# Kernel optimization log

Hardware: AMD Instinct MI355X
Metric: run time of the kernel (lower is better)

## Reference

```python
import jax, jax.numpy as jnp
import numpy as np

# RRFU config (matches init_kwargs)
S = 2          # scale_factor
G = 4          # groups
K = 3          # sample_k
C = 64         # in_channels
B, H, W_IN = 4, 128, 128
SC = S * S     # s_c
KC = K * K     # sample_c (3x3 = 9)


def setup_inputs() -> dict:
    key = jax.random.key(0)
    ks = jax.random.split(key, 9)
    x = jax.random.normal(ks[0], (B, C, H, W_IN), jnp.float32)
    # 1x1 conv weights stored as (out_ch, in_ch); std chosen per module's init
    # (mask convs are zero-init in the original; use small random so math is nontrivial)
    w_off = jax.random.normal(ks[1], (G * SC * 2, C), jnp.float32) * 0.001
    b_off = jnp.zeros((G * SC * 2,), jnp.float32)
    w_offm = jax.random.normal(ks[2], (G * SC * 2, C), jnp.float32) * 0.01
    b_offm = jnp.zeros((G * SC * 2,), jnp.float32)
    w_sk = jax.random.normal(ks[3], (KC, C), jnp.float32) * 0.005
    b_sk = jnp.zeros((KC,), jnp.float32)
    w_km = jax.random.normal(ks[4], (KC, C), jnp.float32) * 0.01
    b_km = jnp.zeros((KC,), jnp.float32)
    return {"x": x, "w_off": w_off, "b_off": b_off, "w_offm": w_offm,
            "b_offm": b_offm, "w_sk": w_sk, "b_sk": b_sk, "w_km": w_km, "b_km": b_km}


def _conv1x1(x, w, b):
    return jnp.einsum('oc,bchw->bohw', w, x) + b[None, :, None, None]


def _bilinear_border(img, iy, ix):
    """img: (Cg,H,W); iy,ix: (Ho,Wo) pixel coords. grid_sample bilinear, padding_mode='border'."""
    Hh, Ww = img.shape[1], img.shape[2]
    ix = jnp.clip(ix, 0.0, Ww - 1.0)
    iy = jnp.clip(iy, 0.0, Hh - 1.0)
    x0 = jnp.floor(ix)
    y0 = jnp.floor(iy)
    wx = ix - x0
    wy = iy - y0
    x0i = x0.astype(jnp.int32)
    y0i = y0.astype(jnp.int32)
    x1i = jnp.minimum(x0i + 1, Ww - 1)
    y1i = jnp.minimum(y0i + 1, Hh - 1)
    v00 = img[:, y0i, x0i]
    v01 = img[:, y0i, x1i]
    v10 = img[:, y1i, x0i]
    v11 = img[:, y1i, x1i]
    return (v00 * (1 - wx) * (1 - wy) + v01 * wx * (1 - wy)
            + v10 * (1 - wx) * wy + v11 * wx * wy)


def reference(x, w_off, b_off, w_offm, b_offm, w_sk, b_sk, w_km, b_km):
    b0, c0, h0, w0 = x.shape
    # learned offsets, gated by sigmoid mask
    off = _conv1x1(x, w_off, b_off) * jax.nn.sigmoid(_conv1x1(x, w_offm, b_offm))
    bg = b0 * G
    # (b, g*S*S*2, h, w) -> (bg, S, S, 2, h, w) -> (bg, h, S, w, S, 2) -> (bg, S*h, S*w, 2)
    off = off.reshape(bg, S, S, 2, h0, w0).transpose(0, 4, 1, 5, 2, 3).reshape(bg, S * h0, S * w0, 2)
    Ho, Wo = S * h0, S * w0
    # coord_base + offset, normalized then un-normalized for align_corners=False grid_sample
    cx = jnp.arange(Wo, dtype=x.dtype) + 0.5
    cy = jnp.arange(Ho, dtype=x.dtype) + 0.5
    ix = (cx[None, None, :] + off[..., 0]) * (w0 / Wo) - 0.5  # (bg, Ho, Wo)
    iy = (cy[None, :, None] + off[..., 1]) * (h0 / Ho) - 0.5
    x_r = x.reshape(bg, c0 // G, h0, w0)
    x_def = jax.vmap(_bilinear_border)(x_r, iy, ix).reshape(b0, c0, Ho, Wo)
    # CARAFE-style dynamic reassembly: softmax kernel over 3x3 neighborhood
    sk = _conv1x1(x_def, w_sk, b_sk) * jax.nn.sigmoid(_conv1x1(x_def, w_km, b_km))
    skn = jax.nn.softmax(sk, axis=1)  # (b, 9, Ho, Wo)
    pad = K // 2
    xp = jnp.pad(x_def, ((0, 0), (0, 0), (pad, pad), (pad, pad)))  # zero pad like F.unfold
    out = jnp.zeros_like(x_def)
    for ky in range(K):  # fixed 3x3 taps; avoids materializing (b,c,9,Ho,Wo)
        for kx in range(K):
            out = out + skn[:, ky * K + kx][:, None] * xp[:, :, ky:ky + Ho, kx:kx + Wo]
    return out
```

## Files before the change

kernel.cpp:

```cpp
#include <hip/hip_runtime.h>
#include <hip/hip_fp16.h>

typedef _Float16 h2 __attribute__((ext_vector_type(2)));

constexpr int Bc  = 4;
constexpr int Cc  = 64;
constexpr int H0  = 128;
constexpr int W0  = 128;
constexpr int HW  = H0 * W0;
constexpr int Gc  = 4;
constexpr int HOc = H0 * 2;
constexpr int WOc = W0 * 2;

constexpr int TW = 16;
constexpr int TH = 8;
constexpr int HX = TW + 2;
constexpr int HY = TH + 2;
constexpr int NHALO = HX * HY;
constexpr int NTASK = Gc * NHALO;

constexpr int SXC = 10;
constexpr int SYC = 6;
constexpr int SN  = SXC * SYC;
constexpr int NPAIR = Cc / 2;

union hu32 { unsigned u; h2 h; };

__device__ __forceinline__ float dot2(h2 a, unsigned bw, float c) {
    hu32 cv; cv.u = bw;
#if __has_builtin(__builtin_amdgcn_fdot2)
    return __builtin_amdgcn_fdot2(a, cv.h, c, false);
#else
    return fmaf((float)a[0], (float)cv.h[0],
                fmaf((float)a[1], (float)cv.h[1], c));
#endif
}

__global__ __launch_bounds__(256) void kT_prep(
    const float* __restrict__ w_off, const float* __restrict__ w_offm,
    const float* __restrict__ w_sk,  const float* __restrict__ w_km,
    __half2* __restrict__ wpk0, __half2* __restrict__ wpk)
{
    const int i = blockIdx.x * 256 + threadIdx.x;
    if (i < 2048) {
        const int c2  = i >> 6;
        const int rem = i & 63;
        const int mat = rem >> 5;
        const int r   = rem & 31;
        const float* src = mat ? w_offm : w_off;
        wpk0[i] = __floats2half2_rn(src[r * Cc + 2 * c2],
                                    src[r * Cc + 2 * c2 + 1]);
    } else if (i < 2048 + 576) {
        const int j   = i - 2048;
        const int mat = j >= 288;
        const int jj  = mat ? j - 288 : j;
        const int k   = jj >> 5;
        const int c2  = jj & 31;
        const float* src = mat ? w_km : w_sk;
        wpk[j] = __floats2half2_rn(src[k * Cc + 2 * c2],
                                   src[k * Cc + 2 * c2 + 1]);
    }
}

__global__ __launch_bounds__(256) void k0_offsets(
    const float* __restrict__ x, const unsigned* __restrict__ wpk0,
    const float* __restrict__ b_off, const float* __restrict__ b_offm,
    __half2* __restrict__ offbuf, unsigned* __restrict__ xt)
{
    const int b    = blockIdx.y;
    const int t    = threadIdx.x;
    const int wave = t >> 6, lane = t & 63;
    const int r0   = __builtin_amdgcn_readfirstlane(wave * 8);
    const int px   = blockIdx.x * 64 + lane;

    float a[8], m[8];
#pragma unroll
    for (int q = 0; q < 8; ++q) { a[q] = 0.f; m[q] = 0.f; }
    unsigned xtr[NPAIR];

    const float*    xp = x + (size_t)b * Cc * HW + px;
    const unsigned* wp = wpk0 + r0;

#pragma unroll 4
    for (int c2 = 0; c2 < NPAIR; ++c2) {
        const float x0 = xp[(2 * c2)     * HW];
        const float x1 = xp[(2 * c2 + 1) * HW];
        hu32 xh; xh.h = h2{(_Float16)x0, (_Float16)x1};
        xtr[c2] = xh.u;
#pragma unroll
        for (int q = 0; q < 8; ++q) {
            a[q] = dot2(xh.h, wp[c2 * 64 + q],      a[q]);
            m[q] = dot2(xh.h, wp[c2 * 64 + 32 + q], m[q]);
        }
    }

    __half2* ob = offbuf + ((size_t)b * HW + px) * 16 + (r0 >> 1);
#pragma unroll
    for (int j = 0; j < 4; ++j) {
        const int r = r0 + 2 * j;
        const float sx = 1.f / (1.f + __expf(-(m[2 * j]     + b_offm[r])));
        const float sy = 1.f / (1.f + __expf(-(m[2 * j + 1] + b_offm[r + 1])));
        const float vx = (a[2 * j]     + b_off[r])     * sx;
        const float vy = (a[2 * j + 1] + b_off[r + 1]) * sy;
        ob[j] = __floats2half2_rn(vx, vy);
    }

    if (wave == 0) {
        unsigned* xo = xt + ((size_t)b * HW + px) * NPAIR;
#pragma unroll
        for (int c2 = 0; c2 < NPAIR; ++c2) xo[c2] = xtr[c2];
    }
}

__global__ __launch_bounds__(256) void k1_fused(
    const unsigned* __restrict__ xt, const __half2* __restrict__ offbuf,
    const unsigned* __restrict__ wsku, const float* __restrict__ b_sk,
    const float* __restrict__ b_km,
    float* __restrict__ out)
{
    __shared__ h2    xd2[NPAIR][NHALO];
    __shared__ float ovl[2304];
    h2*       xstage2 = (h2*)ovl;
    float*    kmb     = ovl;
    unsigned* sknb    = (unsigned*)(ovl + 128 * 9);

    const unsigned* wkmu = wsku + 288;

    const int b    = blockIdx.y;
    const int tile = blockIdx.x;
    const int ox = (tile & 15) * TW;
    const int oy = (tile >> 4) * TH;
    const int t  = threadIdx.x;
    const int syr = (oy >> 1) - 1;
    const int sxr = (ox >> 1) - 1;

    const unsigned* xtb = xt + (size_t)b * HW * NPAIR;
    const __half2*  obb = offbuf + (size_t)b * HW * 16;

    unsigned* xs_u = (unsigned*)xstage2;
    for (int i = t; i < NPAIR * SN; i += 256) {
        const int c2  = i & 31;
        const int pos = i >> 5;
        const int r   = pos / SXC;
        const int j   = pos - r * SXC;
        const int yy  = min(max(syr + r, 0), H0 - 1);
        const int xx  = min(max(sxr + j, 0), W0 - 1);
        xs_u[c2 * SN + pos] = xtb[(yy * W0 + xx) * NPAIR + c2];
    }
    __syncthreads();

    for (int task = t; task < NTASK; task += 256) {
        const int g   = task / NHALO;
        const int pix = task - g * NHALO;
        const int hy  = pix / HX;
        const int hx  = pix - hy * HX;
        const int gy  = oy - 1 + hy;
        const int gx  = ox - 1 + hx;
        if (gy < 0 || gy >= HOc || gx < 0 || gx >= WOc) {
#pragma unroll
            for (int p = 0; p < 8; ++p) xd2[g * 8 + p][pix] = (h2)0;
            continue;
        }
        const int sy = gy & 1, sx = gx & 1;
        const int h  = gy >> 1, w  = gx >> 1;
        const __half2 o2 = obb[(size_t)(h * W0 + w) * 16 + g * 4 + sy * 2 + sx];
        const float offx = __low2float(o2);
        const float offy = __high2float(o2);

        float ix = ((float)gx + 0.5f + offx) * 0.5f - 0.5f;
        float iy = ((float)gy + 0.5f + offy) * 0.5f - 0.5f;
        ix = fminf(fmaxf(ix, 0.f), (float)(W0 - 1));
        iy = fminf(fmaxf(iy, 0.f), (float)(H0 - 1));
        const float x0f = floorf(ix), y0f = floorf(iy);
        const float wx = ix - x0f,   wy = iy - y0f;
        const int x0 = (int)x0f, y0 = (int)y0f;
        const int x1 = min(x0 + 1, W0 - 1), y1 = min(y0 + 1, H0 - 1);
        const float w00 = (1.f - wx) * (1.f - wy);
        const float w01 = wx * (1.f - wy);
        const float w10 = (1.f - wx) * wy;
        const float w11 = wx * wy;

        const int j0 = x0 - sxr, j1 = x1 - sxr;
        const int i0 = y0 - syr, i1 = y1 - syr;
        const bool inl = (j0 >= 0) & (j1 < SXC) & (i0 >= 0) & (i1 < SYC);

        const _Float16 W00 = (_Float16)w00, W01 = (_Float16)w01;
        const _Float16 W10 = (_Float16)w10, W11 = (_Float16)w11;

        if (inl) {
            const int o00 = i0 * SXC + j0, o01 = i0 * SXC + j1;
            const int o10 = i1 * SXC + j0, o11 = i1 * SXC + j1;
            const h2* s2 = xstage2 + (g * 8) * SN;
#pragma unroll
            for (int p = 0; p < 8; ++p) {
                const h2* pc = s2 + p * SN;
                xd2[g * 8 + p][pix] =
                    pc[o00] * W00 + pc[o01] * W01 + pc[o10] * W10 + pc[o11] * W11;
            }
        } else {
            const int o00 = (y0 * W0 + x0) * NPAIR, o01 = (y0 * W0 + x1) * NPAIR;
            const int o10 = (y1 * W0 + x0) * NPAIR, o11 = (y1 * W0 + x1) * NPAIR;
#pragma unroll
            for (int p = 0; p < 8; ++p) {
                const int c2 = g * 8 + p;
                hu32 v00, v01, v10, v11;
                v00.u = xtb[o00 + c2]; v01.u = xtb[o01 + c2];
                v10.u = xtb[o10 + c2]; v11.u = xtb[o11 + c2];
                xd2[c2][pix] =
                    v00.h * W00 + v01.h * W01 + v10.h * W10 + v11.h * W11;
            }
        }
    }
    __syncthreads();

    {
        const int p   = t & 127;
        const int ctr = ((p >> 4) + 1) * HX + (p & 15) + 1;
        h2 xv[NPAIR];
#pragma unroll
        for (int c2 = 0; c2 < NPAIR; ++c2) xv[c2] = xd2[c2][ctr];

        float acc[9];
        if (t < 128) {
#pragma unroll
            for (int k = 0; k < 9; ++k) {
                float a = 0.f;
#pragma unroll
                for (int c2 = 0; c2 < NPAIR; ++c2)
                    a = dot2(xv[c2], wsku[k * 32 + c2], a);
                acc[k] = a;
            }
        } else {
#pragma unroll
            for (int k = 0; k < 9; ++k) {
                float a = 0.f;
#pragma unroll
                for (int c2 = 0; c2 < NPAIR; ++c2)
                    a = dot2(xv[c2], wkmu[k * 32 + c2], a);
                kmb[p * 9 + k] = a;
            }
        }
        __syncthreads();

        if (t < 128) {
            float sv[9], mx = -1e30f;
#pragma unroll
            for (int k = 0; k < 9; ++k) {
                const float z = kmb[p * 9 + k] + b_km[k];
                sv[k] = (acc[k] + b_sk[k]) / (1.f + __expf(-z));
                mx = fmaxf(mx, sv[k]);
            }
            float sum = 0.f;
#pragma unroll
            for (int k = 0; k < 9; ++k) { sv[k] = __expf(sv[k] - mx); sum += sv[k]; }
            const float inv = 1.f / sum;
#pragma unroll
            for (int k = 0; k < 9; ++k) {
                const unsigned hu = __half_as_ushort(__float2half(sv[k] * inv));
                sknb[p * 9 + k] = hu | (hu << 16);
            }
        }
    }
    __syncthreads();

    {
        const int sq    = t & 31;
        const int chunk = t >> 5;
        const int sqx = sq & 7, sqy = sq >> 3;
        const int hx0 = 2 * sqx, hy0 = 2 * sqy;
        const int p00 = (2 * sqy) * TW + 2 * sqx;

        hu32 s00[9], s01[9], s10[9], s11[9];
#pragma unroll
        for (int k = 0; k < 9; ++k) {
            s00[k].u = sknb[p00 * 9 + k];        s01[k].u = sknb[(p00 + 1) * 9 + k];
            s10[k].u = sknb[(p00 + TW) * 9 + k]; s11[k].u = sknb[(p00 + TW + 1) * 9 + k];
        }
        const int orow0 = oy + 2 * sqy, ocol0 = ox + 2 * sqx;

#pragma unroll
        for (int i = 0; i < 4; ++i) {
            const int pr = chunk * 4 + i;
            h2 wd[4][4];
#pragma unroll
            for (int ry = 0; ry < 4; ++ry) {
                const int base = (hy0 + ry) * HX + hx0;
#pragma unroll
                for (int rx = 0; rx < 4; ++rx)
                    wd[ry][rx] = xd2[pr][base + rx];
            }
            h2 a00 = (h2)0, a01 = (h2)0, a10 = (h2)0, a11 = (h2)0;
#pragma unroll
            for (int ky = 0; ky < 3; ++ky)
#pragma unroll
                for (int kx = 0; kx < 3; ++kx) {
                    const int k = ky * 3 + kx;
                    a00 += s00[k].h * wd[ky    ][kx    ];
                    a01 += s01[k].h * wd[ky    ][kx + 1];
                    a10 += s10[k].h * wd[ky + 1][kx    ];
                    a11 += s11[k].h * wd[ky + 1][kx + 1];
                }
            float* ob0 = out + ((size_t)(b * Cc + 2 * pr)) * (HOc * WOc)
                             + (size_t)orow0 * WOc + ocol0;
            float* ob1 = ob0 + (size_t)(HOc * WOc);
            *reinterpret_cast<float2*>(ob0)       = make_float2((float)a00[0], (float)a01[0]);
            *reinterpret_cast<float2*>(ob0 + WOc) = make_float2((float)a10[0], (float)a11[0]);
            *reinterpret_cast<float2*>(ob1)       = make_float2((float)a00[1], (float)a01[1]);
            *reinterpret_cast<float2*>(ob1 + WOc) = make_float2((float)a10[1], (float)a11[1]);
        }
    }
}

extern "C" void kernel_launch(void* const* d_in, const int* in_sizes, int n_in,
                              void* d_out, int out_size, void* d_ws, size_t ws_size,
                              hipStream_t stream)
{
    const float* x      = (const float*)d_in[0];
    const float* w_off  = (const float*)d_in[1];
    const float* b_off  = (const float*)d_in[2];
    const float* w_offm = (const float*)d_in[3];
    const float* b_offm = (const float*)d_in[4];
    const float* w_sk   = (const float*)d_in[5];
    const float* b_sk   = (const float*)d_in[6];
    const float* w_km   = (const float*)d_in[7];
    const float* b_km   = (const float*)d_in[8];
    float* outp = (float*)d_out;

    const size_t off_bytes  = (size_t)Bc * HW * 16 * sizeof(__half2);
    const size_t xt_bytes   = (size_t)Bc * HW * NPAIR * sizeof(unsigned);
    const size_t wpk0_bytes = 2048 * sizeof(__half2);
    const size_t wpk_bytes  = 576 * sizeof(__half2);
    if (ws_size < off_bytes + xt_bytes + wpk0_bytes + wpk_bytes) return;
    __half2*  offbuf = (__half2*)d_ws;
    unsigned* xtbuf  = (unsigned*)((char*)d_ws + off_bytes);
    __half2*  wpk0   = (__half2*)((char*)d_ws + off_bytes + xt_bytes);
    __half2*  wpk    = (__half2*)((char*)d_ws + off_bytes + xt_bytes + wpk0_bytes);

    dim3 blk(256);
    hipLaunchKernelGGL(kT_prep, dim3(11), blk, 0, stream,
                       w_off, w_offm, w_sk, w_km, wpk0, wpk);

    dim3 g0(HW / 64, Bc);
    hipLaunchKernelGGL(k0_offsets, g0, blk, 0, stream,
                       x, (const unsigned*)wpk0, b_off, b_offm, offbuf, xtbuf);

    dim3 g1(512, Bc);
    hipLaunchKernelGGL(k1_fused, g1, blk, 0, stream,
                       xtbuf, offbuf, (const unsigned*)wpk, b_sk, b_km, outp);
}
```

Baseline: 60.71 us.

## Process two vertical tiles per block with register-prefetched staging of second tile

Each block of the fused kernel now handles two stacked 16x8 output tiles, halving the grid. The source staging data for both tiles is loaded into registers up front, and the second tile's copy is written to shared memory after the first tile's sampling phase, hiding global load latency. The staging buffer gets its own shared allocation instead of aliasing the softmax scratch, and the mask logits are kept in half precision. This adds register pressure (16 prefetch registers) and shared memory, which may reduce occupancy, and halves the number of blocks available for parallelism.

Result: faster. 55.43 us (-8.7%).

```diff
diff --git a/kernel.cpp b/kernel.cpp
--- a/kernel.cpp
+++ b/kernel.cpp
@@ -23,6 +23,7 @@
 constexpr int SYC = 6;
 constexpr int SN  = SXC * SYC;
 constexpr int NPAIR = Cc / 2;
+constexpr int NSTG  = NPAIR * SN;
 
 union hu32 { unsigned u; h2 h; };
 
@@ -118,196 +119,229 @@
     const float* __restrict__ b_km,
     float* __restrict__ out)
 {
-    __shared__ h2    xd2[NPAIR][NHALO];
-    __shared__ float ovl[2304];
-    h2*       xstage2 = (h2*)ovl;
-    float*    kmb     = ovl;
-    unsigned* sknb    = (unsigned*)(ovl + 128 * 9);
+    __shared__ h2       xd2[NPAIR][NHALO];
+    __shared__ unsigned xs_u[NSTG];
+    __shared__ unsigned short kmbh[128 * 9];
+    __shared__ unsigned sknb[128 * 9];
 
     const unsigned* wkmu = wsku + 288;
 
     const int b    = blockIdx.y;
-    const int tile = blockIdx.x;
-    const int ox = (tile & 15) * TW;
-    const int oy = (tile >> 4) * TH;
+    const int tp   = blockIdx.x;
+    const int ox = (tp & 15) * TW;
+    const int oyb = (tp >> 4) * (2 * TH);
     const int t  = threadIdx.x;
-    const int syr = (oy >> 1) - 1;
     const int sxr = (ox >> 1) - 1;
+    const int syr0 = (oyb >> 1) - 1;
+    const int syr1 = syr0 + (TH >> 1);
 
     const unsigned* xtb = xt + (size_t)b * HW * NPAIR;
     const __half2*  obb = offbuf + (size_t)b * HW * 16;
 
-    unsigned* xs_u = (unsigned*)xstage2;
-    for (int i = t; i < NPAIR * SN; i += 256) {
-        const int c2  = i & 31;
-        const int pos = i >> 5;
-        const int r   = pos / SXC;
-        const int j   = pos - r * SXC;
-        const int yy  = min(max(syr + r, 0), H0 - 1);
-        const int xx  = min(max(sxr + j, 0), W0 - 1);
-        xs_u[c2 * SN + pos] = xtb[(yy * W0 + xx) * NPAIR + c2];
+    unsigned pre0[8], pre1[8];
+#pragma unroll
+    for (int k = 0; k < 8; ++k) {
+        const int i = t + k * 256;
+        if (i < NSTG) {
+            const int c2  = i & 31;
+            const int pos = i >> 5;
+            const int r   = pos / SXC;
+            const int j   = pos - r * SXC;
+            const int xx  = min(max(sxr + j, 0), W0 - 1);
+            const int yy0 = min(max(syr0 + r, 0), H0 - 1);
+            const int yy1 = min(max(syr1 + r, 0), H0 - 1);
+            pre0[k] = xtb[(yy0 * W0 + xx) * NPAIR + c2];
+            pre1[k] = xtb[(yy1 * W0 + xx) * NPAIR + c2];
+        }
+    }
+#pragma unroll
+    for (int k = 0; k < 8; ++k) {
+        const int i = t + k * 256;
+        if (i < NSTG) {
+            const int c2 = i & 31, pos = i >> 5;
+            xs_u[c2 * SN + pos] = pre0[k];
+        }
     }
     __syncthreads();
 
-    for (int task = t; task < NTASK; task += 256) {
-        const int g   = task / NHALO;
-        const int pix = task - g * NHALO;
-        const int hy  = pix / HX;
-        const int hx  = pix - hy * HX;
-        const int gy  = oy - 1 + hy;
-        const int gx  = ox - 1 + hx;
-        if (gy < 0 || gy >= HOc || gx < 0 || gx >= WOc) {
-#pragma unroll
-            for (int p = 0; p < 8; ++p) xd2[g * 8 + p][pix] = (h2)0;
-            continue;
-        }
-        const int sy = gy & 1, sx = gx & 1;
-        const int h  = gy >> 1, w  = gx >> 1;
-        const __half2 o2 = obb[(size_t)(h * W0 + w) * 16 + g * 4 + sy * 2 + sx];
-        const float offx = __low2float(o2);
-        const float offy = __high2float(o2);
-
-        float ix = ((float)gx + 0.5f + offx) * 0.5f - 0.5f;
-        float iy = ((float)gy + 0.5f + offy) * 0.5f - 0.5f;
-        ix = fminf(fmaxf(ix, 0.f), (float)(W0 - 1));
-        iy = fminf(fmaxf(iy, 0.f), (float)(H0 - 1));
-        const float x0f = floorf(ix), y0f = floorf(iy);
-        const float wx = ix - x0f,   wy = iy - y0f;
-        const int x0 = (int)x0f, y0 = (int)y0f;
-        const int x1 = min(x0 + 1, W0 - 1), y1 = min(y0 + 1, H0 - 1);
-        const float w00 = (1.f - wx) * (1.f - wy);
-        const float w01 = wx * (1.f - wy);
-        const float w10 = (1.f - wx) * wy;
-        const float w11 = wx * wy;
-
-        const int j0 = x0 - sxr, j1 = x1 - sxr;
-        const int i0 = y0 - syr, i1 = y1 - syr;
-        const bool inl = (j0 >= 0) & (j1 < SXC) & (i0 >= 0) & (i1 < SYC);
-
-        const _Float16 W00 = (_Float16)w00, W01 = (_Float16)w01;
-        const _Float16 W10 = (_Float16)w10, W11 = (_Float16)w11;
-
-        if (inl) {
-            const int o00 = i0 * SXC + j0, o01 = i0 * SXC + j1;
-            const int o10 = i1 * SXC + j0, o11 = i1 * SXC + j1;
-            const h2* s2 = xstage2 + (g * 8) * SN;
-#pragma unroll
-            for (int p = 0; p < 8; ++p) {
-                const h2* pc = s2 + p * SN;
-                xd2[g * 8 + p][pix] =
-                    pc[o00] * W00 + pc[o01] * W01 + pc[o10] * W10 + pc[o11] * W11;
-            }
-        } else {
-            const int o00 = (y0 * W0 + x0) * NPAIR, o01 = (y0 * W0 + x1) * NPAIR;
-            const int o10 = (y1 * W0 + x0) * NPAIR, o11 = (y1 * W0 + x1) * NPAIR;
-#pragma unroll
-            for (int p = 0; p < 8; ++p) {
-                const int c2 = g * 8 + p;
-                hu32 v00, v01, v10, v11;
-                v00.u = xtb[o00 + c2]; v01.u = xtb[o01 + c2];
-                v10.u = xtb[o10 + c2]; v11.u = xtb[o11 + c2];
-                xd2[c2][pix] =
-                    v00.h * W00 + v01.h * W01 + v10.h * W10 + v11.h * W11;
-            }
-        }
-    }
-    __syncthreads();
-
-    {
-        const int p   = t & 127;
-        const int ctr = ((p >> 4) + 1) * HX + (p & 15) + 1;
-        h2 xv[NPAIR];
-#pragma unroll
-        for (int c2 = 0; c2 < NPAIR; ++c2) xv[c2] = xd2[c2][ctr];
-
-        float acc[9];
-        if (t < 128) {
+    for (int yt = 0; yt < 2; ++yt) {
+        const int oy  = oyb + yt * TH;
+        const int syr = yt ? syr1 : syr0;
+        const h2* xstage2 = (const h2*)xs_u;
+
+        for (int task = t; task < NTASK; task += 256) {
+            const int g   = task / NHALO;
+            const int pix = task - g * NHALO;
+            const int hy  = pix / HX;
+            const int hx  = pix - hy * HX;
+            const int gy  = oy - 1 + hy;
+            const int gx  = ox - 1 + hx;
+            if (gy < 0 || gy >= HOc || gx < 0 || gx >= WOc) {
+#pragma unroll
+                for (int p = 0; p < 8; ++p) xd2[g * 8 + p][pix] = (h2)0;
+                continue;
+            }
+            const int sy = gy & 1, sx = gx & 1;
+            const int h  = gy >> 1, w  = gx >> 1;
+            const __half2 o2 = obb[(size_t)(h * W0 + w) * 16 + g * 4 + sy * 2 + sx];
+            const float offx = __low2float(o2);
+            const float offy = __high2float(o2);
+
+            float ix = ((float)gx + 0.5f + offx) * 0.5f - 0.5f;
+            float iy = ((float)gy + 0.5f + offy) * 0.5f - 0.5f;
+            ix = fminf(fmaxf(ix, 0.f), (float)(W0 - 1));
+            iy = fminf(fmaxf(iy, 0.f), (float)(H0 - 1));
+            const float x0f = floorf(ix), y0f = floorf(iy);
+            const float wx = ix - x0f,   wy = iy - y0f;
+            const int x0 = (int)x0f, y0 = (int)y0f;
+            const int x1 = min(x0 + 1, W0 - 1), y1 = min(y0 + 1, H0 - 1);
+            const float w00 = (1.f - wx) * (1.f - wy);
+            const float w01 = wx * (1.f - wy);
+            const float w10 = (1.f - wx) * wy;
+            const float w11 = wx * wy;
+
+            const int j0 = x0 - sxr, j1 = x1 - sxr;
+            const int i0 = y0 - syr, i1 = y1 - syr;
+            const bool inl = (j0 >= 0) & (j1 < SXC) & (i0 >= 0) & (i1 < SYC);
+
+            const _Float16 W00 = (_Float16)w00, W01 = (_Float16)w01;
+            const _Float16 W10 = (_Float16)w10, W11 = (_Float16)w11;
+
+            if (inl) {
+                const int o00 = i0 * SXC + j0, o01 = i0 * SXC + j1;
+                const int o10 = i1 * SXC + j0, o11 = i1 * SXC + j1;
+                const h2* s2 = xstage2 + (g * 8) * SN;
+#pragma unroll
+                for (int p = 0; p < 8; ++p) {
+                    const h2* pc = s2 + p * SN;
+                    xd2[g * 8 + p][pix] =
+                        pc[o00] * W00 + pc[o01] * W01 + pc[o10] * W10 + pc[o11] * W11;
+                }
+            } else {
+                const int o00 = (y0 * W0 + x0) * NPAIR, o01 = (y0 * W0 + x1) * NPAIR;
+                const int o10 = (y1 * W0 + x0) * NPAIR, o11 = (y1 * W0 + x1) * NPAIR;
+#pragma unroll
+                for (int p = 0; p < 8; ++p) {
+                    const int c2 = g * 8 + p;
+                    hu32 v00, v01, v10, v11;
+                    v00.u = xtb[o00 + c2]; v01.u = xtb[o01 + c2];
+                    v10.u = xtb[o10 + c2]; v11.u = xtb[o11 + c2];
+                    xd2[c2][pix] =
+                        v00.h * W00 + v01.h * W01 + v10.h * W10 + v11.h * W11;
+                }
+            }
+        }
+        __syncthreads();
+
+        if (yt == 0) {
+#pragma unroll
+            for (int k = 0; k < 8; ++k) {
+                const int i = t + k * 256;
+                if (i < NSTG) {
+                    const int c2 = i & 31, pos = i >> 5;
+                    xs_u[c2 * SN + pos] = pre1[k];
+                }
+            }
+        }
+
+        {
+            const int p   = t & 127;
+            const int ctr = ((p >> 4) + 1) * HX + (p & 15) + 1;
+            h2 xv[NPAIR];
+#pragma unroll
+            for (int c2 = 0; c2 < NPAIR; ++c2) xv[c2] = xd2[c2][ctr];
+
+            float acc[9];
+            if (t < 128) {
+#pragma unroll
+                for (int k = 0; k < 9; ++k) {
+                    float a = 0.f;
+#pragma unroll
+                    for (int c2 = 0; c2 < NPAIR; ++c2)
+                        a = dot2(xv[c2], wsku[k * 32 + c2], a);
+                    acc[k] = a;
+                }
+            } else {
+#pragma unroll
+                for (int k = 0; k < 9; ++k) {
+                    float a = 0.f;
+#pragma unroll
+                    for (int c2 = 0; c2 < NPAIR; ++c2)
+                        a = dot2(xv[c2], wkmu[k * 32 + c2], a);
+                    kmbh[p * 9 + k] = __half_as_ushort(__float2half(a));
+                }
+            }
+            __syncthreads();
+
+            if (t < 128) {
+                float sv[9], mx = -1e30f;
+#pragma unroll
+                for (int k = 0; k < 9; ++k) {
+                    const float z = __half2float(__ushort_as_half(kmbh[p * 9 + k]))
+                                    + b_km[k];
+                    sv[k] = (acc[k] + b_sk[k]) / (1.f + __expf(-z));
+                    mx = fmaxf(mx, sv[k]);
+                }
+                float sum = 0.f;
+#pragma unroll
+                for (int k = 0; k < 9; ++k) { sv[k] = __expf(sv[k] - mx); sum += sv[k]; }
+                const float inv = 1.f / sum;
+#pragma unroll
+                for (int k = 0; k < 9; ++k) {
+                    const unsigned hu = __half_as_ushort(__float2half(sv[k] * inv));
+                    sknb[p * 9 + k] = hu | (hu << 16);
+                }
+            }
+        }
+        __syncthreads();
+
+        {
+            const int sq    = t & 31;
+            const int chunk = t >> 5;
+            const int sqx = sq & 7, sqy = sq >> 3;
+            const int hx0 = 2 * sqx, hy0 = 2 * sqy;
+            const int p00 = (2 * sqy) * TW + 2 * sqx;
+
+            hu32 s00[9], s01[9], s10[9], s11[9];
 #pragma unroll
             for (int k = 0; k < 9; ++k) {
-                float a = 0.f;
-#pragma unroll
-                for (int c2 = 0; c2 < NPAIR; ++c2)
-                    a = dot2(xv[c2], wsku[k * 32 + c2], a);
-                acc[k] = a;
-            }
-        } else {
-#pragma unroll
-            for (int k = 0; k < 9; ++k) {
-                float a = 0.f;
-#pragma unroll
-                for (int c2 = 0; c2 < NPAIR; ++c2)
-                    a = dot2(xv[c2], wkmu[k * 32 + c2], a);
-                kmb[p * 9 + k] = a;
+                s00[k].u = sknb[p00 * 9 + k];        s01[k].u = sknb[(p00 + 1) * 9 + k];
+                s10[k].u = sknb[(p00 + TW) * 9 + k]; s11[k].u = sknb[(p00 + TW + 1) * 9 + k];
+            }
+            const int orow0 = oy + 2 * sqy, ocol0 = ox + 2 * sqx;
+
+#pragma unroll
+            for (int i = 0; i < 4; ++i) {
+                const int pr = chunk * 4 + i;
+                h2 wd[4][4];
+#pragma unroll
+                for (int ry = 0; ry < 4; ++ry) {
+                    const int base = (hy0 + ry) * HX + hx0;
+#pragma unroll
+                    for (int rx = 0; rx < 4; ++rx)
+                        wd[ry][rx] = xd2[pr][base + rx];
+                }
+                h2 a00 = (h2)0, a01 = (h2)0, a10 = (h2)0, a11 = (h2)0;
+#pragma unroll
+                for (int ky = 0; ky < 3; ++ky)
+#pragma unroll
+                    for (int kx = 0; kx < 3; ++kx) {
+                        const int k = ky * 3 + kx;
+                        a00 += s00[k].h * wd[ky    ][kx    ];
+                        a01 += s01[k].h * wd[ky    ][kx + 1];
+                        a10 += s10[k].h * wd[ky + 1][kx    ];
+                        a11 += s11[k].h * wd[ky + 1][kx + 1];
+                    }
+                float* ob0 = out + ((size_t)(b * Cc + 2 * pr)) * (HOc * WOc)
+                                 + (size_t)orow0 * WOc + ocol0;
+                float* ob1 = ob0 + (size_t)(HOc * WOc);
+                *reinterpret_cast<float2*>(ob0)       = make_float2((float)a00[0], (float)a01[0]);
+                *reinterpret_cast<float2*>(ob0 + WOc) = make_float2((float)a10[0], (float)a11[0]);
+                *reinterpret_cast<float2*>(ob1)       = make_float2((float)a00[1], (float)a01[1]);
+                *reinterpret_cast<float2*>(ob1 + WOc) = make_float2((float)a10[1], (float)a11[1]);
             }
         }
         __syncthreads();
-
-        if (t < 128) {
-            float sv[9], mx = -1e30f;
-#pragma unroll
-            for (int k = 0; k < 9; ++k) {
-                const float z = kmb[p * 9 + k] + b_km[k];
-                sv[k] = (acc[k] + b_sk[k]) / (1.f + __expf(-z));
-                mx = fmaxf(mx, sv[k]);
-            }
-            float sum = 0.f;
-#pragma unroll
-            for (int k = 0; k < 9; ++k) { sv[k] = __expf(sv[k] - mx); sum += sv[k]; }
-            const float inv = 1.f / sum;
-#pragma unroll
-            for (int k = 0; k < 9; ++k) {
-                const unsigned hu = __half_as_ushort(__float2half(sv[k] * inv));
-                sknb[p * 9 + k] = hu | (hu << 16);
-            }
-        }
-    }
-    __syncthreads();
-
-    {
-        const int sq    = t & 31;
-        const int chunk = t >> 5;
-        const int sqx = sq & 7, sqy = sq >> 3;
-        const int hx0 = 2 * sqx, hy0 = 2 * sqy;
-        const int p00 = (2 * sqy) * TW + 2 * sqx;
-
-        hu32 s00[9], s01[9], s10[9], s11[9];
-#pragma unroll
-        for (int k = 0; k < 9; ++k) {
-            s00[k].u = sknb[p00 * 9 + k];        s01[k].u = sknb[(p00 + 1) * 9 + k];
-            s10[k].u = sknb[(p00 + TW) * 9 + k]; s11[k].u = sknb[(p00 + TW + 1) * 9 + k];
-        }
-        const int orow0 = oy + 2 * sqy, ocol0 = ox + 2 * sqx;
-
-#pragma unroll
-        for (int i = 0; i < 4; ++i) {
-            const int pr = chunk * 4 + i;
-            h2 wd[4][4];
-#pragma unroll
-            for (int ry = 0; ry < 4; ++ry) {
-                const int base = (hy0 + ry) * HX + hx0;
-#pragma unroll
-                for (int rx = 0; rx < 4; ++rx)
-                    wd[ry][rx] = xd2[pr][base + rx];
-            }
-            h2 a00 = (h2)0, a01 = (h2)0, a10 = (h2)0, a11 = (h2)0;
-#pragma unroll
-            for (int ky = 0; ky < 3; ++ky)
-#pragma unroll
-                for (int kx = 0; kx < 3; ++kx) {
-                    const int k = ky * 3 + kx;
-                    a00 += s00[k].h * wd[ky    ][kx    ];
-                    a01 += s01[k].h * wd[ky    ][kx + 1];
-                    a10 += s10[k].h * wd[ky + 1][kx    ];
-                    a11 += s11[k].h * wd[ky + 1][kx + 1];
-                }
-            float* ob0 = out + ((size_t)(b * Cc + 2 * pr)) * (HOc * WOc)
-                             + (size_t)orow0 * WOc + ocol0;
-            float* ob1 = ob0 + (size_t)(HOc * WOc);
-            *reinterpret_cast<float2*>(ob0)       = make_float2((float)a00[0], (float)a01[0]);
-            *reinterpret_cast<float2*>(ob0 + WOc) = make_float2((float)a10[0], (float)a11[0]);
-            *reinterpret_cast<float2*>(ob1)       = make_float2((float)a00[1], (float)a01[1]);
-            *reinterpret_cast<float2*>(ob1 + WOc) = make_float2((float)a10[1], (float)a11[1]);
-        }
     }
 }
 
@@ -344,7 +378,7 @@
     hipLaunchKernelGGL(k0_offsets, g0, blk, 0, stream,
                        x, (const unsigned*)wpk0, b_off, b_offm, offbuf, xtbuf);
 
-    dim3 g1(512, Bc);
+    dim3 g1(256, Bc);
     hipLaunchKernelGGL(k1_fused, g1, blk, 0, stream,
                        xtbuf, offbuf, (const unsigned*)wpk, b_sk, b_km, outp);
 }
```
